# Optimization experiments

Hardware: AMD Instinct MI355X
Metric: run time of the kernel (lower is better)

## Reference

```python
import jax, jax.numpy as jnp
import numpy as np

R, S, M, K = 512, 48, 4096, 16
RADIUS = 4.0 * 0.025
DIMS = [511, 256, 256, 256, 3]


def posenc(x, n_freqs):
    freqs = 2.0 ** jnp.arange(n_freqs, dtype=x.dtype)
    xf = x[..., None, :] * freqs[:, None]            # [..., F, C]
    sc = jnp.stack([jnp.sin(xf), jnp.cos(xf)], -2)   # [..., F, 2, C]
    return jnp.concatenate([x, sc.reshape(x.shape[:-1] + (-1,))], -1)


def ball_query(q, p, radius, k):
    # pytorch3d-style: first k points (by index order) within radius.
    # dists are squared distances, 0 for padding; neighbors are 0 for padding; idx -1 for padding.
    d2 = jnp.sum((q[:, None, :] - p[None, :, :]) ** 2, -1)    # [Nq, M]
    m = p.shape[0]
    order = jnp.where(d2 < radius * radius, jnp.arange(m), m)
    neg, idx = jax.lax.top_k(-order, k)                        # k smallest valid indices
    valid = neg > -m
    dists = jnp.where(valid, jnp.take_along_axis(d2, idx, axis=1), 0.0)
    nbrs = jnp.where(valid[..., None], p[idx], 0.0)
    return dists, jnp.where(valid, idx, -1), nbrs


def setup_inputs() -> dict:
    key = jax.random.key(0)
    ks = jax.random.split(key, 16)
    inp = {
        "points": jax.random.uniform(ks[0], (R, S, 3), jnp.float32),
        "normals": jax.random.normal(ks[1], (R * S, 3), jnp.float32),
        "view_dirs": jax.random.normal(ks[2], (R * S, 3), jnp.float32),
        "feature_vectors": jax.random.normal(ks[3], (R * S, 256), jnp.float32),
        "indices": 0,
        "physical_particles": jax.random.uniform(ks[4], (M, 3), jnp.float32),
        "rays": jax.random.normal(ks[5], (R, 6), jnp.float32),
        "ro": jax.random.normal(ks[6], (1, 3), jnp.float32),
    }
    for l in range(4):
        scale = (2.0 / DIMS[l + 1]) ** 0.5
        inp[f"W{l}"] = jax.random.normal(ks[7 + l], (DIMS[l + 1], DIMS[l]), jnp.float32) * scale
        inp[f"b{l}"] = jnp.zeros((DIMS[l + 1],), jnp.float32)
    return inp


def reference(points, normals, view_dirs, feature_vectors, indices, physical_particles,
              rays, ro, W0, b0, W1, b1, W2, b2, W3, b3):
    q = points.reshape(-1, 3)                                     # [R*S, 3]
    dists, idx, nbrs = ball_query(q, physical_particles, RADIUS, K)
    dists = dists.reshape(R, S, K)
    nbrs = nbrs.reshape(R, S, K, 3)
    nn_mask = dists != 0                                          # padded entries have dist 0
    num_nn = nn_mask.sum(-1, keepdims=True)                       # [R, S, 1]

    hit_pos_emb = posenc(q, 10)                                   # [R*S, 63]
    hit_dir_emb = jnp.repeat(posenc(rays[:, 3:], 4), S, axis=0)   # [R*S, 27]

    # smoothing_position (exclude_ray=True)
    dn = jnp.linalg.norm(nbrs - points[:, :, None, :], axis=-1)   # [R, S, K]
    w = jnp.maximum(1.0 - (dn / RADIUS) ** 3, 0.0)
    density = w.sum(-1, keepdims=True)                            # [R, S, 1]
    smoothed = (w[..., None] * nbrs).sum(-2) / (density + 1e-12)  # [R, S, 3]

    sp = smoothed.reshape(-1, 3)
    dirs = sp - ro
    dirs = dirs / jnp.linalg.norm(dirs, axis=-1, keepdims=True)

    density_emb = posenc(density.reshape(-1, 1), 4)               # [R*S, 9]
    smoothed_pos_emb = posenc(sp, 10)                             # [R*S, 63]

    # masked variance of neighbor offsets
    diff = jnp.where(nn_mask[..., None], nbrs - points[:, :, None, :], 0.0)
    mean = diff.sum(-2) / (num_nn + 1e-12)
    var = jnp.where(nn_mask[..., None], (diff - mean[:, :, None, :]) ** 2, 0.0).sum(-2) / (num_nn + 1e-12)
    var_emb = posenc(var.reshape(-1, 3), 10)                      # [R*S, 63]

    x = jnp.concatenate([hit_pos_emb, density_emb, smoothed_pos_emb, var_emb,
                         hit_dir_emb, posenc(dirs, 4), normals, feature_vectors], -1)  # [R*S, 511]

    for Wl, bl in ((W0, b0), (W1, b1), (W2, b2)):
        x = jax.nn.relu(x @ Wl.T + bl)
    return jax.nn.sigmoid(x @ W3.T + b3)
```

## Files before the change

### kernel.cpp

```cpp
#include <hip/hip_runtime.h>

typedef _Float16 f16;
typedef f16 f16x8 __attribute__((ext_vector_type(8)));
typedef float f32x4 __attribute__((ext_vector_type(4)));
typedef unsigned short u16;

__device__ __forceinline__ void glds16(const void* g, void* l) {
  __builtin_amdgcn_global_load_lds(
      (const __attribute__((address_space(1))) unsigned*)g,
      (__attribute__((address_space(3))) unsigned*)l, 16, 0, 0);
}


struct FT {
  u16 v[256];
  static constexpr u16 enc(int s, int f, int k) {
    return (u16)(s | (f << 5) | (k << 9));
  }
  constexpr void p3(int base, int F, int src) {
    v[base + 0] = enc(src + 0, 0, 0);
    v[base + 1] = enc(src + 1, 0, 0);
    v[base + 2] = enc(src + 2, 0, 0);
    for (int f = 0; f < F; ++f)
      for (int r = 0; r < 6; ++r) {
        int comp = (r < 3) ? r : r - 3;
        v[base + 3 + f * 6 + r] = enc(src + comp, f, (r < 3) ? 1 : 2);
      }
  }
  constexpr void p1(int base, int F, int src) {
    v[base] = enc(src, 0, 0);
    for (int f = 0; f < F; ++f) {
      v[base + 1 + 2 * f] = enc(src, f, 1);
      v[base + 2 + 2 * f] = enc(src, f, 2);
    }
  }
  constexpr FT() : v{} {
    p3(0, 10, 0);
    p1(63, 4, 3);
    p3(72, 10, 4);
    p3(135, 10, 7);
    p3(198, 4, 10);
    p3(225, 4, 13);
    v[252] = enc(16, 0, 0);
    v[253] = enc(17, 0, 0);
    v[254] = enc(18, 0, 0);
    v[255] = enc(0, 0, 3);
  }
};
__constant__ FT ftab = FT();

__device__ float4 g_sorted[4096];
__device__ int    g_cellStart[1001];

__global__ __launch_bounds__(1024) void build_grid(const float* __restrict__ parts)
{
  __shared__ int cnt[1000];
  __shared__ int pos[1000];
  __shared__ int wpre[125];
  const int tid = threadIdx.x;
  for (int j = tid; j < 1000; j += 1024) cnt[j] = 0;
  __syncthreads();

  float px[4], py[4], pz[4];
  int cd[4];
  #pragma unroll
  for (int t = 0; t < 4; ++t) {
    int i = tid + t * 1024;
    float x = parts[3 * i], y = parts[3 * i + 1], z = parts[3 * i + 2];
    int cx = min(max((int)(x * 10.0f), 0), 9);
    int cy = min(max((int)(y * 10.0f), 0), 9);
    int cz = min(max((int)(z * 10.0f), 0), 9);
    cd[t] = (cz * 10 + cy) * 10 + cx;
    px[t] = x; py[t] = y; pz[t] = z;
    atomicAdd(&cnt[cd[t]], 1);
  }
  __syncthreads();

  if (tid < 125) {
    int s = 0;
    #pragma unroll
    for (int k = 0; k < 8; ++k) s += cnt[tid * 8 + k];
    wpre[tid] = s;
  }
  __syncthreads();
  if (tid == 0) {
    int s = 0;
    for (int c = 0; c < 125; ++c) { int t = wpre[c]; wpre[c] = s; s += t; }
  }
  __syncthreads();
  if (tid < 125) {
    int run = wpre[tid];
    #pragma unroll
    for (int k = 0; k < 8; ++k) {
      int c = tid * 8 + k;
      int n = cnt[c];
      pos[c] = run;
      g_cellStart[c] = run;
      run += n;
    }
  }
  if (tid == 0) g_cellStart[1000] = 4096;
  __syncthreads();

  #pragma unroll
  for (int t = 0; t < 4; ++t) {
    int p = atomicAdd(&pos[cd[t]], 1);
    g_sorted[p] = make_float4(px[t], py[t], pz[t], __int_as_float(tid + t * 1024));
  }
}

__global__ __launch_bounds__(256) void prep_weights(
    const float* __restrict__ W0, const float* __restrict__ W1,
    const float* __restrict__ W2,
    f16* __restrict__ w0f, f16* __restrict__ w1f, f16* __restrict__ w2f)
{
  int i = blockIdx.x * 256 + threadIdx.x;
  float v; f16* pf; int n, c;
  if (i < 131072) {
    n = i >> 9; c = i & 511;
    v = (c < 255) ? W0[n * 511 + c] : ((c == 255) ? 0.0f : W0[n * 511 + (c - 1)]);
    pf = w0f;
  } else if (i < 196608) {
    int j = i - 131072; n = j >> 8; c = j & 255; v = W1[j]; pf = w1f;
  } else {
    int j = i - 196608; n = j >> 8; c = j & 255; v = W2[j]; pf = w2f;
  }
  int kt = c >> 5, g = (c >> 3) & 3, jj = c & 7;
  int u = n * 4 + (g ^ ((n >> 1) & 3));
  pf[kt * 8192 + u * 8 + jj] = (f16)v;
}

#define MAXCH 5

__global__ __launch_bounds__(256) void feat_kernel(
    const float* __restrict__ points, const float* __restrict__ normals,
    const float* __restrict__ parts, const float* __restrict__ rays,
    const float* __restrict__ ro, f16* __restrict__ Xf)
{
  __shared__ float sdata[4][20];

  const int tid = threadIdx.x;
  const int lane = tid & 63, wv = tid >> 6;
  const int q = blockIdx.x * 4 + wv;
  const float qx = points[3 * q], qy = points[3 * q + 1], qz = points[3 * q + 2];
  const float RQ = 0.1f * 0.1f;

  int nAcc = 0;
  float sdx = 0, sdy = 0, sdz = 0;
  float s2x = 0, s2y = 0, s2z = 0;
  float sw = 0, swx = 0, swy = 0, swz = 0;

  const int cqx = min(max((int)(qx * 10.0f), 0), 9);
  const int cqy = min(max((int)(qy * 10.0f), 0), 9);
  const int cqz = min(max((int)(qz * 10.0f), 0), 9);

  int st_l = 0, cn_l = 0;
  if (lane < 9) {
    int dz = lane / 3, dy = lane - dz * 3;
    int cz = cqz - 1 + dz, cy = cqy - 1 + dy;
    if ((unsigned)cz <= 9u && (unsigned)cy <= 9u) {
      int x0 = max(cqx - 1, 0), x1 = min(cqx + 1, 9);
      int rb = (cz * 10 + cy) * 10;
      st_l = g_cellStart[rb + x0];
      cn_l = g_cellStart[rb + x1 + 1] - st_l;
    }
  }

  int pk[9], bk[9];
  int run = 0;
  #pragma unroll
  for (int k = 0; k < 9; ++k) {
    int stk = __builtin_amdgcn_readlane(st_l, k);
    int cnk = __builtin_amdgcn_readlane(cn_l, k);
    pk[k] = run;
    bk[k] = stk - run;
    run += cnk;
  }
  const int C = run;
  const bool fb = (C > MAXCH * 64);

  if (!fb) {
    float4 sv[MAXCH];
    int iv[MAXCH];
    unsigned long long hm[MAXCH];
    #pragma unroll
    for (int ch = 0; ch < MAXCH; ++ch) {
      if (ch * 64 < C) {
        int s = ch * 64 + lane;
        int g = bk[0];
        #pragma unroll
        for (int k = 1; k < 9; ++k) g = (s >= pk[k]) ? bk[k] : g;
        float4 pt = g_sorted[min(g + s, 4095)];
        if (s >= C) {
          pt.x = 1e9f; pt.y = 1e9f; pt.z = 1e9f;
          pt.w = __int_as_float(0x7fffffff);
        }
        sv[ch] = pt;
        iv[ch] = __float_as_int(pt.w);
        float ex = pt.x - qx, ey = pt.y - qy, ez = pt.z - qz;
        float d2 = __fadd_rn(__fadd_rn(__fmul_rn(ex, ex), __fmul_rn(ey, ey)),
                             __fmul_rn(ez, ez));
        hm[ch] = __ballot(d2 < RQ);
      } else {
        hm[ch] = 0ULL;
      }
    }

    int N = 0;
    #pragma unroll
    for (int ch = 0; ch < MAXCH; ++ch) N += __popcll(hm[ch]);

    int thr = 0x7fffffff;
    if (N > 16) {
      int lo = 0, hi = 4095;
      while (lo < hi) {
        int mid = (lo + hi) >> 1;
        int c = 0;
        #pragma unroll
        for (int ch = 0; ch < MAXCH; ++ch)
          if (ch * 64 < C)
            c += __popcll(hm[ch] & __ballot(iv[ch] <= mid));
        if (c >= 16) hi = mid; else lo = mid + 1;
      }
      thr = lo;
    }

    #pragma unroll
    for (int ch = 0; ch < MAXCH; ++ch) {
      if (ch * 64 < C) {
        float4 pt = sv[ch];
        float ex = pt.x - qx, ey = pt.y - qy, ez = pt.z - qz;
        float d2 = __fadd_rn(__fadd_rn(__fmul_rn(ex, ex), __fmul_rn(ey, ey)),
                             __fmul_rn(ez, ez));
        if (d2 < RQ && iv[ch] <= thr) {
          nAcc++;
          sdx += ex; sdy += ey; sdz += ez;
          s2x += ex * ex; s2y += ey * ey; s2z += ez * ez;
          float dn = sqrtf(d2);
          float t = dn * 10.0f;
          float w = fmaxf(1.0f - t * t * t, 0.0f);
          sw += w; swx += w * pt.x; swy += w * pt.y; swz += w * pt.z;
        }
      }
    }
  } else {
    int total = 0;
    for (int jr = 0; jr < 64; ++jr) {
      int pi = jr * 64 + lane;
      float x = parts[3 * pi], y = parts[3 * pi + 1], z = parts[3 * pi + 2];
      float ex = x - qx, ey = y - qy, ez = z - qz;
      float d2 = __fadd_rn(__fadd_rn(__fmul_rn(ex, ex), __fmul_rn(ey, ey)),
                           __fmul_rn(ez, ez));
      bool hit = d2 < RQ;
      unsigned long long m = __ballot(hit);
      int pos = __builtin_amdgcn_mbcnt_hi((unsigned)(m >> 32),
                __builtin_amdgcn_mbcnt_lo((unsigned)m, 0u));
      if (hit && (total + pos < 16)) {
        nAcc++;
        sdx += ex; sdy += ey; sdz += ez;
        s2x += ex * ex; s2y += ey * ey; s2z += ez * ez;
        float dn = sqrtf(d2);
        float t = dn * 10.0f;
        float w = fmaxf(1.0f - t * t * t, 0.0f);
        sw += w; swx += w * x; swy += w * y; swz += w * z;
      }
      total += __popcll(m);
      if (total >= 16) break;
    }
  }

  #define WRED(x) { _Pragma("unroll") for (int o = 32; o; o >>= 1) x += __shfl_xor(x, o, 64); }
  float fn = (float)nAcc;
  WRED(fn); WRED(sdx); WRED(sdy); WRED(sdz);
  WRED(s2x); WRED(s2y); WRED(s2z);
  WRED(sw); WRED(swx); WRED(swy); WRED(swz);
  #undef WRED

  float tq = sqrtf(qx * qx + qy * qy + qz * qz) * 10.0f;
  float wpad = fmaxf(1.0f - tq * tq * tq, 0.0f);
  float density = sw + (16.0f - fn) * wpad;
  float invd = 1.0f / (density + 1e-12f);
  float spx = swx * invd, spy = swy * invd, spz = swz * invd;

  float invn = 1.0f / (fn + 1e-12f);
  float mx = sdx * invn, my = sdy * invn, mz = sdz * invn;
  float vx = fmaxf((s2x - 2.0f * mx * sdx + fn * mx * mx) * invn, 0.0f);
  float vy = fmaxf((s2y - 2.0f * my * sdy + fn * my * my) * invn, 0.0f);
  float vz = fmaxf((s2z - 2.0f * mz * sdz + fn * mz * mz) * invn, 0.0f);

  float dxx = spx - ro[0], dyy = spy - ro[1], dzz = spz - ro[2];
  float il = 1.0f / sqrtf(dxx * dxx + dyy * dyy + dzz * dzz);

  if (lane == 0) {
    float* s = sdata[wv];
    s[0] = qx; s[1] = qy; s[2] = qz; s[3] = density;
    s[4] = spx; s[5] = spy; s[6] = spz;
    s[7] = vx; s[8] = vy; s[9] = vz;
    int r = q / 48;
    s[10] = rays[6 * r + 3]; s[11] = rays[6 * r + 4]; s[12] = rays[6 * r + 5];
    s[13] = dxx * il; s[14] = dyy * il; s[15] = dzz * il;
    s[16] = normals[3 * q]; s[17] = normals[3 * q + 1]; s[18] = normals[3 * q + 2];
  }
  __syncthreads();

  const int b = q / 48, m48 = q % 48;
  const size_t base = (size_t)b * 12288;
  #pragma unroll
  for (int it = 0; it < 4; ++it) {
    int c = it * 64 + lane;
    int e = ftab.v[c];
    float sv_ = sdata[wv][e & 31];
    float arg = sv_ * (float)(1 << ((e >> 5) & 15));
    float sn, cs;
    sincosf(arg, &sn, &cs);
    int kind = e >> 9;
    float val = (kind == 0) ? sv_ : (kind == 1 ? sn : (kind == 2 ? cs : 0.0f));
    int kt = c >> 5, g = (c >> 3) & 3, j = c & 7;
    int u = m48 * 4 + (g ^ ((m48 >> 1) & 3));
    Xf[base + kt * 1536 + u * 8 + j] = (f16)val;
  }
}

__global__ __launch_bounds__(256, 2) void fused_mlp(
    const f16* __restrict__ Xf, const float* __restrict__ fvec,
    const f16* __restrict__ w0f, const f16* __restrict__ w1f,
    const f16* __restrict__ w2f,
    const float* __restrict__ b0, const float* __restrict__ b1,
    const float* __restrict__ b2,
    const float* __restrict__ W3, const float* __restrict__ b3,
    float* __restrict__ out)
{
  extern __shared__ char lds[];
  f16* Hf    = (f16*)lds;
  f16* Bs    = (f16*)(lds + 24576);
  f16* Ah_st = (f16*)lds;
  float* w3s = (float*)(lds + 24576);

  const int tid = threadIdx.x, lane = tid & 63, wn = tid >> 6;
  const int l15 = lane & 15, l4 = lane >> 4;
  const int blk = blockIdx.x;

  if (blk & 1) __builtin_amdgcn_s_sleep(8);

  f32x4 acc[3][4];

  const f16* Xft = Xf + (size_t)blk * 12288;

  auto stageB = [&](const f16* wf, int kt) {
    #pragma unroll
    for (int s = 0; s < 4; ++s) {
      int ch = wn + s * 4;
      glds16(wf + kt * 8192 + ch * 512 + lane * 8, Bs + ch * 512 + lane * 8);
    }
  };
  auto stageA = [&](int kt) {
    if (kt < 8) {
      if (wn < 3)
        glds16(Xft + kt * 1536 + wn * 512 + lane * 8, Ah_st + wn * 512 + lane * 8);
    } else {
      if (tid < 192) {
        int m = tid >> 2, g = tid & 3;
        const float* src = fvec + (size_t)(blk * 48 + m) * 256 + (kt - 8) * 32 + g * 8;
        float4 v0 = ((const float4*)src)[0];
        float4 v1 = ((const float4*)src)[1];
        f16 hs[8] = {(f16)v0.x, (f16)v0.y, (f16)v0.z, (f16)v0.w,
                     (f16)v1.x, (f16)v1.y, (f16)v1.z, (f16)v1.w};
        int u = m * 4 + (g ^ ((m >> 1) & 3));
        *(uint4*)(Ah_st + u * 8) = *(uint4*)hs;
      }
    }
  };
  auto bfrags = [&](f16x8* bf) {
    #pragma unroll
    for (int j = 0; j < 4; ++j) {
      int n = wn * 64 + j * 16 + l15;
      int u = n * 4 + (l4 ^ ((n >> 1) & 3));
      bf[j] = __builtin_bit_cast(f16x8, *(const uint4*)(Bs + u * 8));
    }
  };
  auto mfmas = [&](f16x8* af, f16x8* bf) {
    #pragma unroll
    for (int i = 0; i < 3; ++i)
      #pragma unroll
      for (int j = 0; j < 4; ++j)
        acc[i][j] = __builtin_amdgcn_mfma_f32_16x16x32_f16(af[i], bf[j], acc[i][j], 0, 0, 0);
  };
  auto epilogue = [&](const float* bias_) {
    float bv[4];
    #pragma unroll
    for (int j = 0; j < 4; ++j) bv[j] = bias_[wn * 64 + j * 16 + l15];
    #pragma unroll
    for (int i = 0; i < 3; ++i) {
      #pragma unroll
      for (int r = 0; r < 4; ++r) {
        int m = i * 16 + l4 * 4 + r;
        #pragma unroll
        for (int j = 0; j < 4; ++j) {
          int n = wn * 64 + j * 16 + l15;
          float v = fmaxf(acc[i][j][r] + bv[j], 0.0f);
          int u = m * 32 + ((n >> 3) ^ ((m >> 1) & 7));
          Hf[u * 8 + (n & 7)] = (f16)v;
        }
      }
    }
  };

  #pragma unroll
  for (int i = 0; i < 3; ++i)
    #pragma unroll
    for (int j = 0; j < 4; ++j) acc[i][j] = (f32x4){0, 0, 0, 0};

  stageA(0);
  stageB(w0f, 0);
  for (int kt = 0; kt < 16; ++kt) {
    __syncthreads();
    f16x8 af[3], bf[4];
    #pragma unroll
    for (int i = 0; i < 3; ++i) {
      int m = i * 16 + l15;
      int u = m * 4 + (l4 ^ ((m >> 1) & 3));
      af[i] = __builtin_bit_cast(f16x8, *(const uint4*)(Ah_st + u * 8));
    }
    bfrags(bf);
    __syncthreads();
    if (kt < 15) { stageA(kt + 1); stageB(w0f, kt + 1); }
    mfmas(af, bf);
  }
  epilogue(b0);

  #pragma unroll 1
  for (int layer = 0; layer < 2; ++layer) {
    const f16* wf = layer ? w2f : w1f;
    #pragma unroll
    for (int i = 0; i < 3; ++i)
      #pragma unroll
      for (int j = 0; j < 4; ++j) acc[i][j] = (f32x4){0, 0, 0, 0};

    stageB(wf, 0);
    for (int kt = 0; kt < 8; ++kt) {
      __syncthreads();
      f16x8 af[3], bf[4];
      #pragma unroll
      for (int i = 0; i < 3; ++i) {
        int m = i * 16 + l15;
        int g = kt * 4 + l4;
        int u = m * 32 + (g ^ ((m >> 1) & 7));
        af[i] = __builtin_bit_cast(f16x8, *(const uint4*)(Hf + u * 8));
      }
      bfrags(bf);
      __syncthreads();
      if (kt < 7) stageB(wf, kt + 1);
      mfmas(af, bf);
    }
    epilogue(layer ? b2 : b1);
  }

  __syncthreads();
  for (int i = tid; i < 768; i += 256) w3s[i] = W3[i];
  __syncthreads();

  const float B30 = b3[0], B31 = b3[1], B32 = b3[2];
  #pragma unroll 1
  for (int rr = 0; rr < 12; ++rr) {
    int m = wn * 12 + rr;
    int g = lane >> 1, j0 = (lane & 1) * 4;
    int u = m * 32 + (g ^ ((m >> 1) & 7));
    uint2 pk = *(const uint2*)(Hf + u * 8 + j0);
    f16 h4[4];
    *(uint2*)h4 = pk;
    float h0 = (float)h4[0], h1 = (float)h4[1], h2 = (float)h4[2], h3 = (float)h4[3];
    int kc = lane * 4;
    float4 wa = *(const float4*)(w3s + kc);
    float4 wb = *(const float4*)(w3s + 256 + kc);
    float4 wc = *(const float4*)(w3s + 512 + kc);
    float p0 = fmaf(h3, wa.w, fmaf(h2, wa.z, fmaf(h1, wa.y, h0 * wa.x)));
    float p1 = fmaf(h3, wb.w, fmaf(h2, wb.z, fmaf(h1, wb.y, h0 * wb.x)));
    float p2 = fmaf(h3, wc.w, fmaf(h2, wc.z, fmaf(h1, wc.y, h0 * wc.x)));
    #pragma unroll
    for (int o = 32; o; o >>= 1) {
      p0 += __shfl_xor(p0, o, 64);
      p1 += __shfl_xor(p1, o, 64);
      p2 += __shfl_xor(p2, o, 64);
    }
    if (lane == 0) {
      size_t ro_ = (size_t)(blk * 48 + m) * 3;
      out[ro_ + 0] = 1.0f / (1.0f + expf(-(p0 + B30)));
      out[ro_ + 1] = 1.0f / (1.0f + expf(-(p1 + B31)));
      out[ro_ + 2] = 1.0f / (1.0f + expf(-(p2 + B32)));
    }
  }
}

extern "C" void kernel_launch(void* const* d_in, const int* in_sizes, int n_in,
                              void* d_out, int out_size, void* d_ws, size_t ws_size,
                              hipStream_t stream) {
  const float* points  = (const float*)d_in[0];
  const float* normals = (const float*)d_in[1];
  const float* fvec    = (const float*)d_in[3];
  const float* parts   = (const float*)d_in[5];
  const float* rays    = (const float*)d_in[6];
  const float* ro      = (const float*)d_in[7];
  const float* W0 = (const float*)d_in[8];
  const float* b0 = (const float*)d_in[9];
  const float* W1 = (const float*)d_in[10];
  const float* b1 = (const float*)d_in[11];
  const float* W2 = (const float*)d_in[12];
  const float* b2 = (const float*)d_in[13];
  const float* W3 = (const float*)d_in[14];
  const float* b3 = (const float*)d_in[15];

  char* ws = (char*)d_ws;
  f16* Xf  = (f16*)(ws);
  f16* w0f = (f16*)(ws + 12582912);
  f16* w1f = (f16*)(ws + 12845056);
  f16* w2f = (f16*)(ws + 12976128);
  float* out = (float*)d_out;

  (void)hipFuncSetAttribute((const void*)fused_mlp,
                            hipFuncAttributeMaxDynamicSharedMemorySize, 40960);

  build_grid<<<1, 1024, 0, stream>>>(parts);
  prep_weights<<<1024, 256, 0, stream>>>(W0, W1, W2, w0f, w1f, w2f);
  feat_kernel<<<6144, 256, 0, stream>>>(points, normals, parts, rays, ro, Xf);
  fused_mlp<<<512, 256, 40960, stream>>>(Xf, fvec, w0f, w1f, w2f,
                                         b0, b1, b2, W3, b3, out);
}
```

Before: 166.1 us.

## Stage full A tile in LDS once and stream weights directly into registers

The fused MLP kernel now loads the whole 48x512 input tile (precomputed features plus converted feature vectors) into LDS in one pass. Weight fragments are read straight from global memory into registers with one-step register double-buffering, replacing the per-k-tile LDS staging of weights and its two barriers per iteration. Hidden activations ping-pong between two LDS buffers, which removes the intermediate syncs. The block-parity sleep is dropped. The cost is a larger LDS footprint (72KB per block, which may lower blocks per CU) and more global/L2 traffic for weights, since each wave reads them independently.

Result: slower. 173.5 us (+4.5%).

```diff
diff --git a/kernel.cpp b/kernel.cpp
--- a/kernel.cpp
+++ b/kernel.cpp
@@ -331,52 +331,42 @@
     float* __restrict__ out)
 {
   extern __shared__ char lds[];
-  f16* Hf    = (f16*)lds;
-  f16* Bs    = (f16*)(lds + 24576);
-  f16* Ah_st = (f16*)lds;
-  float* w3s = (float*)(lds + 24576);
+  f16* As = (f16*)lds;
+  f16* H2 = (f16*)lds;
+  f16* Hf = (f16*)(lds + 49152);
+  float* w3s = (float*)(lds + 28672);
 
   const int tid = threadIdx.x, lane = tid & 63, wn = tid >> 6;
   const int l15 = lane & 15, l4 = lane >> 4;
   const int blk = blockIdx.x;
 
-  if (blk & 1) __builtin_amdgcn_s_sleep(8);
-
   f32x4 acc[3][4];
 
   const f16* Xft = Xf + (size_t)blk * 12288;
 
-  auto stageB = [&](const f16* wf, int kt) {
-    #pragma unroll
-    for (int s = 0; s < 4; ++s) {
-      int ch = wn + s * 4;
-      glds16(wf + kt * 8192 + ch * 512 + lane * 8, Bs + ch * 512 + lane * 8);
-    }
+  int uB[4];
+  #pragma unroll
+  for (int j = 0; j < 4; ++j) {
+    int n = wn * 64 + j * 16 + l15;
+    uB[j] = n * 4 + (l4 ^ ((n >> 1) & 3));
+  }
+  int uA[3];
+  #pragma unroll
+  for (int i = 0; i < 3; ++i) {
+    int m = i * 16 + l15;
+    uA[i] = m * 4 + (l4 ^ ((m >> 1) & 3));
+  }
+
+  auto zacc = [&]() {
+    #pragma unroll
+    for (int i = 0; i < 3; ++i)
+      #pragma unroll
+      for (int j = 0; j < 4; ++j) acc[i][j] = (f32x4){0, 0, 0, 0};
   };
-  auto stageA = [&](int kt) {
-    if (kt < 8) {
-      if (wn < 3)
-        glds16(Xft + kt * 1536 + wn * 512 + lane * 8, Ah_st + wn * 512 + lane * 8);
-    } else {
-      if (tid < 192) {
-        int m = tid >> 2, g = tid & 3;
-        const float* src = fvec + (size_t)(blk * 48 + m) * 256 + (kt - 8) * 32 + g * 8;
-        float4 v0 = ((const float4*)src)[0];
-        float4 v1 = ((const float4*)src)[1];
-        f16 hs[8] = {(f16)v0.x, (f16)v0.y, (f16)v0.z, (f16)v0.w,
-                     (f16)v1.x, (f16)v1.y, (f16)v1.z, (f16)v1.w};
-        int u = m * 4 + (g ^ ((m >> 1) & 3));
-        *(uint4*)(Ah_st + u * 8) = *(uint4*)hs;
-      }
-    }
-  };
-  auto bfrags = [&](f16x8* bf) {
-    #pragma unroll
-    for (int j = 0; j < 4; ++j) {
-      int n = wn * 64 + j * 16 + l15;
-      int u = n * 4 + (l4 ^ ((n >> 1) & 3));
-      bf[j] = __builtin_bit_cast(f16x8, *(const uint4*)(Bs + u * 8));
-    }
+  auto loadB = [&](const f16* wf, int kt, f16x8* bf) {
+    #pragma unroll
+    for (int j = 0; j < 4; ++j)
+      bf[j] = *(const f16x8*)(wf + kt * 8192 + uB[j] * 8);
   };
   auto mfmas = [&](f16x8* af, f16x8* bf) {
     #pragma unroll
@@ -385,7 +375,7 @@
       for (int j = 0; j < 4; ++j)
         acc[i][j] = __builtin_amdgcn_mfma_f32_16x16x32_f16(af[i], bf[j], acc[i][j], 0, 0, 0);
   };
-  auto epilogue = [&](const float* bias_) {
+  auto epilogue = [&](const float* bias_, f16* Hdst) {
     float bv[4];
     #pragma unroll
     for (int j = 0; j < 4; ++j) bv[j] = bias_[wn * 64 + j * 16 + l15];
@@ -399,61 +389,93 @@
           int n = wn * 64 + j * 16 + l15;
           float v = fmaxf(acc[i][j][r] + bv[j], 0.0f);
           int u = m * 32 + ((n >> 3) ^ ((m >> 1) & 7));
-          Hf[u * 8 + (n & 7)] = (f16)v;
+          Hdst[u * 8 + (n & 7)] = (f16)v;
         }
       }
     }
   };
 
   #pragma unroll
-  for (int i = 0; i < 3; ++i)
-    #pragma unroll
-    for (int j = 0; j < 4; ++j) acc[i][j] = (f32x4){0, 0, 0, 0};
-
-  stageA(0);
-  stageB(w0f, 0);
-  for (int kt = 0; kt < 16; ++kt) {
-    __syncthreads();
-    f16x8 af[3], bf[4];
-    #pragma unroll
-    for (int i = 0; i < 3; ++i) {
-      int m = i * 16 + l15;
-      int u = m * 4 + (l4 ^ ((m >> 1) & 3));
-      af[i] = __builtin_bit_cast(f16x8, *(const uint4*)(Ah_st + u * 8));
-    }
-    bfrags(bf);
-    __syncthreads();
-    if (kt < 15) { stageA(kt + 1); stageB(w0f, kt + 1); }
-    mfmas(af, bf);
-  }
-  epilogue(b0);
-
-  #pragma unroll 1
-  for (int layer = 0; layer < 2; ++layer) {
-    const f16* wf = layer ? w2f : w1f;
-    #pragma unroll
-    for (int i = 0; i < 3; ++i)
-      #pragma unroll
-      for (int j = 0; j < 4; ++j) acc[i][j] = (f32x4){0, 0, 0, 0};
-
-    stageB(wf, 0);
+  for (int r = 0; r < 6; ++r)
+    glds16(Xft + r * 2048 + tid * 8, As + r * 2048 + tid * 8);
+  if (tid < 192) {
+    int m = tid >> 2, g = tid & 3;
+    int u = m * 4 + (g ^ ((m >> 1) & 3));
+    #pragma unroll
+    for (int kf = 0; kf < 8; ++kf) {
+      const float* src = fvec + (size_t)(blk * 48 + m) * 256 + kf * 32 + g * 8;
+      float4 v0 = ((const float4*)src)[0];
+      float4 v1 = ((const float4*)src)[1];
+      f16 hs[8] = {(f16)v0.x, (f16)v0.y, (f16)v0.z, (f16)v0.w,
+                   (f16)v1.x, (f16)v1.y, (f16)v1.z, (f16)v1.w};
+      *(uint4*)(As + (8 + kf) * 1536 + u * 8) = *(uint4*)hs;
+    }
+  }
+  __syncthreads();
+
+  zacc();
+  {
+    f16x8 bf[4], bfn[4];
+    loadB(w0f, 0, bf);
+    #pragma unroll
+    for (int kt = 0; kt < 16; ++kt) {
+      if (kt < 15) loadB(w0f, kt + 1, bfn);
+      f16x8 af[3];
+      #pragma unroll
+      for (int i = 0; i < 3; ++i)
+        af[i] = *(const f16x8*)(As + kt * 1536 + uA[i] * 8);
+      mfmas(af, bf);
+      #pragma unroll
+      for (int j = 0; j < 4; ++j) bf[j] = bfn[j];
+    }
+  }
+  epilogue(b0, Hf);
+  __syncthreads();
+
+  zacc();
+  {
+    f16x8 bf[4], bfn[4];
+    loadB(w1f, 0, bf);
+    #pragma unroll
     for (int kt = 0; kt < 8; ++kt) {
-      __syncthreads();
-      f16x8 af[3], bf[4];
+      if (kt < 7) loadB(w1f, kt + 1, bfn);
+      f16x8 af[3];
       #pragma unroll
       for (int i = 0; i < 3; ++i) {
         int m = i * 16 + l15;
         int g = kt * 4 + l4;
         int u = m * 32 + (g ^ ((m >> 1) & 7));
-        af[i] = __builtin_bit_cast(f16x8, *(const uint4*)(Hf + u * 8));
-      }
-      bfrags(bf);
-      __syncthreads();
-      if (kt < 7) stageB(wf, kt + 1);
+        af[i] = *(const f16x8*)(Hf + u * 8);
+      }
       mfmas(af, bf);
-    }
-    epilogue(layer ? b2 : b1);
-  }
+      #pragma unroll
+      for (int j = 0; j < 4; ++j) bf[j] = bfn[j];
+    }
+  }
+  epilogue(b1, H2);
+  __syncthreads();
+
+  zacc();
+  {
+    f16x8 bf[4], bfn[4];
+    loadB(w2f, 0, bf);
+    #pragma unroll
+    for (int kt = 0; kt < 8; ++kt) {
+      if (kt < 7) loadB(w2f, kt + 1, bfn);
+      f16x8 af[3];
+      #pragma unroll
+      for (int i = 0; i < 3; ++i) {
+        int m = i * 16 + l15;
+        int g = kt * 4 + l4;
+        int u = m * 32 + (g ^ ((m >> 1) & 7));
+        af[i] = *(const f16x8*)(H2 + u * 8);
+      }
+      mfmas(af, bf);
+      #pragma unroll
+      for (int j = 0; j < 4; ++j) bf[j] = bfn[j];
+    }
+  }
+  epilogue(b2, Hf);
 
   __syncthreads();
   for (int i = tid; i < 768; i += 256) w3s[i] = W3[i];
@@ -517,11 +539,11 @@
   float* out = (float*)d_out;
 
   (void)hipFuncSetAttribute((const void*)fused_mlp,
-                            hipFuncAttributeMaxDynamicSharedMemorySize, 40960);
+                            hipFuncAttributeMaxDynamicSharedMemorySize, 73728);
 
   build_grid<<<1, 1024, 0, stream>>>(parts);
   prep_weights<<<1024, 256, 0, stream>>>(W0, W1, W2, w0f, w1f, w2f);
   feat_kernel<<<6144, 256, 0, stream>>>(points, normals, parts, rays, ro, Xf);
-  fused_mlp<<<512, 256, 40960, stream>>>(Xf, fvec, w0f, w1f, w2f,
+  fused_mlp<<<512, 256, 73728, stream>>>(Xf, fvec, w0f, w1f, w2f,
                                          b0, b1, b2, W3, b3, out);
 }
```
